# Optimization experiments

Hardware: AMD Instinct MI355X
Metric: run time of the kernel (lower is better)

The kernel has to match this reference:

```python
import jax, jax.numpy as jnp
import numpy as np

HID = 128
NLAYERS = 8
LAT = 32
DIM_IN = 63 + 15 + LAT  # pe(xyz,L=10)=3+60, pe(shift,L=2)=3+12, latent=32 -> 110


def _pe(x, L):
    # NeRF positional encoding, include_input=True, freq-major [sin3,cos3] per freq
    freqs = (2.0 ** jnp.arange(L)).astype(x.dtype)
    xf = x[..., None, :] * freqs[:, None]                      # [..., L, 3]
    sc = jnp.concatenate([jnp.sin(xf), jnp.cos(xf)], axis=-1)  # [..., L, 6]
    return jnp.concatenate([x, sc.reshape(*x.shape[:-1], 6 * L)], axis=-1)


def setup_inputs() -> dict:
    key = jax.random.key(0)
    ks = jax.random.split(key, 24)
    B, P, V = 2, 32768, 5023
    d = {}
    d["pts"] = jax.random.normal(ks[0], (B, P, 3), jnp.float32)
    d["deformed_mesh_pts"] = jax.random.normal(ks[1], (B, V, 3), jnp.float32)
    d["cano_verts"] = jax.random.normal(ks[2], (1, V, 3), jnp.float32)
    d["motion_latent"] = jax.random.normal(ks[3], (B, P, LAT), jnp.float32)
    for i in range(NLAYERS):
        fin = DIM_IN if i == 0 else (DIM_IN + HID if i == NLAYERS // 2 else HID)
        d[f"w{i}"] = jax.random.normal(ks[4 + i], (HID, fin), jnp.float32) / np.sqrt(fin).astype(np.float32)
        d[f"b{i}"] = jnp.zeros((HID,), jnp.float32)
    d["w_out"] = jax.random.normal(ks[20], (3, HID), jnp.float32) * 0.01
    d["b_out"] = jnp.zeros((3,), jnp.float32)
    return d


def reference(pts, deformed_mesh_pts, cano_verts, motion_latent,
              w0, b0, w1, b1, w2, b2, w3, b3, w4, b4, w5, b5, w6, b6, w7, b7,
              w_out, b_out):
    # mesh-guided shift per vertex
    mesh_shift = cano_verts - deformed_mesh_pts                 # [B,V,3]
    # point-to-point NN search (squared euclidean cdist + argmin)
    d2 = ((pts ** 2).sum(-1)[:, :, None]
          + (deformed_mesh_pts ** 2).sum(-1)[:, None, :]
          - 2.0 * jnp.einsum('bpc,bvc->bpv', pts, deformed_mesh_pts))  # [B,P,V]
    d2 = jnp.maximum(d2, 0.0)
    idx = jnp.argmin(d2, axis=-1)                               # [B,P]
    dist = jnp.min(d2, axis=-1)                                 # [B,P]
    weight = jnp.exp(-dist)[..., None]                          # 1/exp(dist)
    gidx = jnp.broadcast_to(idx[:, :, None], idx.shape + (3,))
    gshift = jnp.take_along_axis(mesh_shift, gidx, axis=1) * weight  # [B,P,3]
    # deformation MLP with skip connection at layer 4
    initial = jnp.concatenate([_pe(pts, 10), _pe(gshift, 2), motion_latent], axis=-1)
    ws = [w0, w1, w2, w3, w4, w5, w6, w7]
    bs = [b0, b1, b2, b3, b4, b5, b6, b7]
    x = initial
    last_feat = x
    for i in range(NLAYERS):
        inp = jnp.concatenate([initial, x], axis=-1) if i == NLAYERS // 2 else x
        x = inp @ ws[i].T + bs[i]
        last_feat = x  # pre-activation feature (out_feat_ls[-1])
        x = jax.nn.relu(x)
    mlp_shift = x @ w_out.T + b_out                             # [B,P,3]
    pts_shifts = gshift + mlp_shift
    return pts + pts_shifts, last_feat
```

## Files before the change

kernel.cpp:

```cpp
#include <hip/hip_runtime.h>
#include <math.h>

typedef unsigned short ushort_t;
typedef unsigned int   uint_t;
typedef __attribute__((ext_vector_type(8)))  short bf16x8;
typedef __attribute__((ext_vector_type(16))) float f32x16;

#define NPTS   65536
#define NV     5023
#define LATD   32
#define KF     110
#define FSTR   112

__device__ __forceinline__ ushort_t f2bf(float f) {
  union { float f; unsigned u; } x; x.f = f;
  unsigned r = x.u + 0x7fffu + ((x.u >> 16) & 1u);
  return (ushort_t)(r >> 16);
}
__device__ __forceinline__ float bf2f(ushort_t u) {
  union { unsigned u; float f; } x; x.u = ((unsigned)u) << 16;
  return x.f;
}
__device__ __forceinline__ uint_t packsplit(float v) {
  const ushort_t h = f2bf(v);
  const ushort_t l = f2bf(v - bf2f(h));
  return (uint_t)h | ((uint_t)l << 16);
}


__global__ __launch_bounds__(256, 4) void k_nnfeat(
    const float* __restrict__ pts, const float* __restrict__ dm,
    const float* __restrict__ cano, const float* __restrict__ lat,
    const float* __restrict__ w0, const float* __restrict__ w1,
    const float* __restrict__ w2, const float* __restrict__ w3,
    const float* __restrict__ w4, const float* __restrict__ w5,
    const float* __restrict__ w6, const float* __restrict__ w7,
    uint_t* __restrict__ feat, float* __restrict__ base3,
    ushort_t* __restrict__ wsWh, ushort_t* __restrict__ wsWl)
{
  const int tid = threadIdx.x;

  if (tid < 144) {
    const int e = blockIdx.x * 144 + tid;
    const int p = e >> 14, local = e & 16383;
    const int n = local >> 7, k = local & 127;
    float v;
    if (p == 0)      v = (k < KF) ? w0[n*110 + k] : 0.f;
    else if (p == 1) v = w1[n*128 + k];
    else if (p == 2) v = w2[n*128 + k];
    else if (p == 3) v = w3[n*128 + k];
    else if (p == 4) v = (k < KF) ? w4[n*238 + k] : 0.f;
    else if (p == 5) v = w4[n*238 + KF + k];
    else if (p == 6) v = w5[n*128 + k];
    else if (p == 7) v = w6[n*128 + k];
    else             v = w7[n*128 + k];
    const ushort_t h = f2bf(v);
    wsWh[e] = h;
    wsWl[e] = f2bf(v - bf2f(h));
  }

  __shared__ float4 sV[512];
  __shared__ float  sD[64];
  __shared__ int    sI[64];

  const int lane = tid & 63, w = tid >> 6;
  const int slot = lane >> 4, s = lane & 15;
  const int g0 = blockIdx.x * 64;
  const int b  = blockIdx.x >> 9;
  const float* __restrict__ dmb = dm + b * NV * 3;
  const int pbase = g0 + w*16 + slot*4;

  float px[4], py[4], pz[4], p2[4], bs[4]; int bi[4];
  #pragma unroll
  for (int j = 0; j < 4; ++j) {
    px[j] = pts[(pbase+j)*3+0]; py[j] = pts[(pbase+j)*3+1]; pz[j] = pts[(pbase+j)*3+2];
    p2[j] = fmaf(px[j],px[j], fmaf(py[j],py[j], pz[j]*pz[j]));
    bs[j] = 3.4e38f; bi[j] = 0;
  }

  for (int v0 = 0; v0 < NV; v0 += 512) {
    __syncthreads();
    #pragma unroll
    for (int it = 0; it < 2; ++it) {
      const int i = it*256 + tid;
      const int v = v0 + i;
      float4 t;
      if (v < NV) {
        const float x = dmb[v*3+0], y = dmb[v*3+1], z = dmb[v*3+2];
        t = make_float4(x, y, z, fmaf(x,x, fmaf(y,y, z*z)));
      } else {
        t = make_float4(0.f, 0.f, 0.f, __builtin_inff());
      }
      sV[i] = t;
    }
    __syncthreads();
    #pragma unroll 8
    for (int k = 0; k < 32; ++k) {
      const float4 t = sV[k*16 + s];
      const int vi = v0 + k*16 + s;
      #pragma unroll
      for (int j = 0; j < 4; ++j) {
        const float dot = fmaf(px[j], t.x, fmaf(py[j], t.y, pz[j]*t.z));
        float d2 = fmaf(-2.f, dot, p2[j] + t.w);
        d2 = fmaxf(d2, 0.f);
        if (d2 < bs[j]) { bs[j] = d2; bi[j] = vi; }
      }
    }
  }

  #pragma unroll
  for (int off = 1; off <= 8; off <<= 1) {
    #pragma unroll
    for (int j = 0; j < 4; ++j) {
      const float ob = __shfl_xor(bs[j], off, 64);
      const int   oi = __shfl_xor(bi[j], off, 64);
      const bool take = (ob < bs[j]) || ((ob == bs[j]) && (oi < bi[j]));
      if (take) { bs[j] = ob; bi[j] = oi; }
    }
  }
  if (s == 0) {
    #pragma unroll
    for (int j = 0; j < 4; ++j) {
      sD[w*16 + slot*4 + j] = bs[j];
      sI[w*16 + slot*4 + j] = bi[j];
    }
  }
  __syncthreads();

  const int p = tid & 63, slice = tid >> 6;
  const int g = g0 + p;
  const float wd = sD[p];
  const int   wi = sI[p];

  const float qx = pts[g*3+0], qy = pts[g*3+1], qz = pts[g*3+2];
  const float wgt = expf(-wd);
  const float sx = (cano[wi*3+0] - dmb[wi*3+0]) * wgt;
  const float sy = (cano[wi*3+1] - dmb[wi*3+1]) * wgt;
  const float sz = (cano[wi*3+2] - dmb[wi*3+2]) * wgt;

  uint_t* __restrict__ fr = feat + (size_t)g * FSTR;

  if (slice == 0) {
    base3[g*3+0] = qx + sx; base3[g*3+1] = qy + sy; base3[g*3+2] = qz + sz;
    fr[0] = packsplit(qx); fr[1] = packsplit(qy); fr[2] = packsplit(qz);
    #pragma unroll
    for (int f = 0; f < 3; ++f) {
      const float F = (float)(1 << f);
      float s0,c0,s1,c1,s2,c2;
      sincosf(qx*F,&s0,&c0); sincosf(qy*F,&s1,&c1); sincosf(qz*F,&s2,&c2);
      const int k = 3 + 6*f;
      fr[k+0]=packsplit(s0); fr[k+1]=packsplit(s1); fr[k+2]=packsplit(s2);
      fr[k+3]=packsplit(c0); fr[k+4]=packsplit(c1); fr[k+5]=packsplit(c2);
    }
    fr[110] = 0; fr[111] = 0;
  } else if (slice == 1) {
    #pragma unroll
    for (int f = 3; f < 7; ++f) {
      const float F = (float)(1 << f);
      float s0,c0,s1,c1,s2,c2;
      sincosf(qx*F,&s0,&c0); sincosf(qy*F,&s1,&c1); sincosf(qz*F,&s2,&c2);
      const int k = 3 + 6*f;
      fr[k+0]=packsplit(s0); fr[k+1]=packsplit(s1); fr[k+2]=packsplit(s2);
      fr[k+3]=packsplit(c0); fr[k+4]=packsplit(c1); fr[k+5]=packsplit(c2);
    }
  } else if (slice == 2) {
    #pragma unroll
    for (int f = 7; f < 10; ++f) {
      const float F = (float)(1 << f);
      float s0,c0,s1,c1,s2,c2;
      sincosf(qx*F,&s0,&c0); sincosf(qy*F,&s1,&c1); sincosf(qz*F,&s2,&c2);
      const int k = 3 + 6*f;
      fr[k+0]=packsplit(s0); fr[k+1]=packsplit(s1); fr[k+2]=packsplit(s2);
      fr[k+3]=packsplit(c0); fr[k+4]=packsplit(c1); fr[k+5]=packsplit(c2);
    }
    #pragma unroll
    for (int j = 0; j < 16; ++j) fr[78+j] = packsplit(lat[g*LATD + j]);
  } else {
    fr[63]=packsplit(sx); fr[64]=packsplit(sy); fr[65]=packsplit(sz);
    #pragma unroll
    for (int f = 0; f < 2; ++f) {
      const float F = (float)(1 << f);
      float s0,c0,s1,c1,s2,c2;
      sincosf(sx*F,&s0,&c0); sincosf(sy*F,&s1,&c1); sincosf(sz*F,&s2,&c2);
      const int k = 66 + 6*f;
      fr[k+0]=packsplit(s0); fr[k+1]=packsplit(s1); fr[k+2]=packsplit(s2);
      fr[k+3]=packsplit(c0); fr[k+4]=packsplit(c1); fr[k+5]=packsplit(c2);
    }
    #pragma unroll
    for (int j = 16; j < 32; ++j) fr[78+j] = packsplit(lat[g*LATD + j]);
  }
}


__device__ __forceinline__ void stage_X(uint_t* __restrict__ sX,
    const uint_t* __restrict__ feat, int g0, int tid)
{
  #pragma unroll
  for (int it = 0; it < 14; ++it) {
    const int idx = it*256 + tid;
    const int m = idx / 28, kc = idx - m*28;
    *(uint4*)(sX + m*136 + kc*4) = *(const uint4*)(feat + (size_t)(g0 + m)*FSTR + kc*4);
  }
  const uint4 z = {0,0,0,0};
  #pragma unroll
  for (int it = 0; it < 2; ++it) {
    const int idx = it*256 + tid;
    const int m = idx >> 2, q = idx & 3;
    *(uint4*)(sX + m*136 + 112 + q*4) = z;
  }
}

__device__ __forceinline__ void zero_acc(f32x16 (&acc)[2][2]) {
  #pragma unroll
  for (int i = 0; i < 2; ++i)
    #pragma unroll
    for (int j = 0; j < 2; ++j)
      acc[i][j] = (f32x16)(0.f);
}

__device__ __forceinline__ void mfma_panel(f32x16 (&acc)[2][2],
    const uint_t* __restrict__ sX,
    const ushort_t* __restrict__ gWh, const ushort_t* __restrict__ gWl,
    int mq, int nq, int l31, int lh)
{
  const int kh = lh*8;
  bf16x8 bh[2], bl[2], nbh[2], nbl[2];
  #pragma unroll
  for (int tn = 0; tn < 2; ++tn) {
    const int n = nq*64 + tn*32 + l31;
    bh[tn] = *(const bf16x8*)(gWh + n*128 + kh);
    bl[tn] = *(const bf16x8*)(gWl + n*128 + kh);
  }
  #pragma unroll
  for (int ks = 0; ks < 8; ++ks) {
    const int ko = ks*16 + kh;
    if (ks < 7) {
      #pragma unroll
      for (int tn = 0; tn < 2; ++tn) {
        const int n = nq*64 + tn*32 + l31;
        nbh[tn] = *(const bf16x8*)(gWh + n*128 + ko + 16);
        nbl[tn] = *(const bf16x8*)(gWl + n*128 + ko + 16);
      }
    }
    bf16x8 ah[2], al[2];
    #pragma unroll
    for (int tm = 0; tm < 2; ++tm) {
      const int m = mq*64 + tm*32 + l31;
      const uint4 ua = *(const uint4*)(sX + m*136 + ko);
      const uint4 ub = *(const uint4*)(sX + m*136 + ko + 4);
      union { uint_t u[4]; bf16x8 v; } H, L;
      H.u[0] = (ua.x & 0xffffu) | (ua.y << 16);
      H.u[1] = (ua.z & 0xffffu) | (ua.w << 16);
      H.u[2] = (ub.x & 0xffffu) | (ub.y << 16);
      H.u[3] = (ub.z & 0xffffu) | (ub.w << 16);
      L.u[0] = (ua.x >> 16) | (ua.y & 0xffff0000u);
      L.u[1] = (ua.z >> 16) | (ua.w & 0xffff0000u);
      L.u[2] = (ub.x >> 16) | (ub.y & 0xffff0000u);
      L.u[3] = (ub.z >> 16) | (ub.w & 0xffff0000u);
      ah[tm] = H.v; al[tm] = L.v;
    }
    #pragma unroll
    for (int tm = 0; tm < 2; ++tm)
      #pragma unroll
      for (int tn = 0; tn < 2; ++tn) {
        acc[tm][tn] = __builtin_amdgcn_mfma_f32_32x32x16_bf16(ah[tm], bh[tn], acc[tm][tn], 0,0,0);
        acc[tm][tn] = __builtin_amdgcn_mfma_f32_32x32x16_bf16(al[tm], bh[tn], acc[tm][tn], 0,0,0);
        acc[tm][tn] = __builtin_amdgcn_mfma_f32_32x32x16_bf16(ah[tm], bl[tn], acc[tm][tn], 0,0,0);
      }
    if (ks < 7) {
      #pragma unroll
      for (int tn = 0; tn < 2; ++tn) { bh[tn] = nbh[tn]; bl[tn] = nbl[tn]; }
    }
  }
}

__device__ __forceinline__ void epi_relu(f32x16 (&acc)[2][2], uint_t* __restrict__ sX,
    const float* __restrict__ bias, int mq, int nq, int l31, int lh)
{
  #pragma unroll
  for (int tm = 0; tm < 2; ++tm)
    #pragma unroll
    for (int tn = 0; tn < 2; ++tn) {
      const int n = nq*64 + tn*32 + l31;
      const float bv = bias[n];
      #pragma unroll
      for (int r = 0; r < 16; ++r) {
        const int row = (r & 3) + 8*(r >> 2) + 4*lh;
        const int m = mq*64 + tm*32 + row;
        const float v = fmaxf(acc[tm][tn][r] + bv, 0.f);
        const ushort_t h = f2bf(v);
        const ushort_t l = f2bf(v - bf2f(h));
        sX[m*136 + n] = (uint_t)h | ((uint_t)l << 16);
      }
    }
}

__global__ __launch_bounds__(256, 2) void k_mlp(
    const uint_t* __restrict__ feat, const float* __restrict__ base3,
    const ushort_t* __restrict__ wsWh, const ushort_t* __restrict__ wsWl,
    const float* __restrict__ b0, const float* __restrict__ b1,
    const float* __restrict__ b2, const float* __restrict__ b3,
    const float* __restrict__ b4, const float* __restrict__ b5,
    const float* __restrict__ b6, const float* __restrict__ b7,
    const float* __restrict__ w_out, const float* __restrict__ b_out,
    float* __restrict__ out)
{
  __shared__ __align__(16) uint_t sX[128*136];
  __shared__ float sB[8*128 + 384 + 4];

  const int tid  = threadIdx.x;
  const int lane = tid & 63, wid = tid >> 6;
  const int l31 = lane & 31, lh = lane >> 5;
  const int mq = wid & 1, nq = wid >> 1;
  const int g0 = blockIdx.x * 128;

  f32x16 acc[2][2];

  stage_X(sX, feat, g0, tid);
  {
    const float* bs[8] = {b0,b1,b2,b3,b4,b5,b6,b7};
    if (tid < 128) {
      #pragma unroll
      for (int l = 0; l < 8; ++l) sB[l*128 + tid] = bs[l][tid];
    }
    for (int i = tid; i < 384; i += 256) sB[1024 + i] = w_out[i];
    if (tid < 3) sB[1408 + tid] = b_out[tid];
  }
  __syncthreads();

  zero_acc(acc);
  mfma_panel(acc, sX, wsWh + 0, wsWl + 0, mq, nq, l31, lh);
  __syncthreads();
  epi_relu(acc, sX, sB + 0, mq, nq, l31, lh);

  for (int l = 1; l <= 3; ++l) {
    __syncthreads();
    zero_acc(acc);
    mfma_panel(acc, sX, wsWh + l*16384, wsWl + l*16384, mq, nq, l31, lh);
    __syncthreads();
    epi_relu(acc, sX, sB + l*128, mq, nq, l31, lh);
  }

  __syncthreads();
  zero_acc(acc);
  mfma_panel(acc, sX, wsWh + 5*16384, wsWl + 5*16384, mq, nq, l31, lh);
  __syncthreads();
  stage_X(sX, feat, g0, tid);
  __syncthreads();
  mfma_panel(acc, sX, wsWh + 4*16384, wsWl + 4*16384, mq, nq, l31, lh);
  __syncthreads();
  epi_relu(acc, sX, sB + 4*128, mq, nq, l31, lh);

  for (int l = 5; l <= 6; ++l) {
    __syncthreads();
    zero_acc(acc);
    mfma_panel(acc, sX, wsWh + (l+1)*16384, wsWl + (l+1)*16384, mq, nq, l31, lh);
    __syncthreads();
    epi_relu(acc, sX, sB + l*128, mq, nq, l31, lh);
  }

  __syncthreads();
  zero_acc(acc);
  mfma_panel(acc, sX, wsWh + 8*16384, wsWl + 8*16384, mq, nq, l31, lh);

  float* __restrict__ out1 = out + (size_t)NPTS*3;
  #pragma unroll
  for (int tm = 0; tm < 2; ++tm)
    #pragma unroll
    for (int tn = 0; tn < 2; ++tn) {
      const int n = nq*64 + tn*32 + l31;
      const float bv = sB[7*128 + n];
      #pragma unroll
      for (int r = 0; r < 16; ++r) {
        const int row = (r & 3) + 8*(r >> 2) + 4*lh;
        const int m = mq*64 + tm*32 + row;
        const float v = acc[tm][tn][r] + bv;
        out1[(size_t)(g0 + m)*128 + n] = v;
        acc[tm][tn][r] = fmaxf(v, 0.f);
      }
    }

  __syncthreads();
  float* __restrict__ sF = (float*)sX;
  #pragma unroll
  for (int tm = 0; tm < 2; ++tm)
    #pragma unroll
    for (int tn = 0; tn < 2; ++tn) {
      const int n = nq*64 + tn*32 + l31;
      #pragma unroll
      for (int r = 0; r < 16; ++r) {
        const int row = (r & 3) + 8*(r >> 2) + 4*lh;
        const int m = mq*64 + tm*32 + row;
        sF[m*132 + n] = acc[tm][tn][r];
      }
    }
  __syncthreads();

  for (int pair = tid; pair < 384; pair += 256) {
    const int m = pair / 3, c = pair - m*3;
    const float* __restrict__ xr = sF + m*132;
    const float* __restrict__ wc = sB + 1024 + c*128;
    float a = 0.f;
    #pragma unroll 8
    for (int k = 0; k < 128; ++k) a = fmaf(xr[k], wc[k], a);
    const int g = g0 + m;
    out[g*3 + c] = base3[g*3 + c] + a + sB[1408 + c];
  }
}

extern "C" void kernel_launch(void* const* d_in, const int* in_sizes, int n_in,
                              void* d_out, int out_size, void* d_ws, size_t ws_size,
                              hipStream_t stream)
{
  const float* pts  = (const float*)d_in[0];
  const float* dm   = (const float*)d_in[1];
  const float* cano = (const float*)d_in[2];
  const float* lat  = (const float*)d_in[3];
  const float* w[8]; const float* b[8];
  for (int i = 0; i < 8; ++i) {
    w[i] = (const float*)d_in[4 + 2*i];
    b[i] = (const float*)d_in[5 + 2*i];
  }
  const float* w_out = (const float*)d_in[20];
  const float* b_out = (const float*)d_in[21];
  float* out = (float*)d_out;

  uint_t*   feat  = (uint_t*)d_ws;
  float*    base3 = (float*)((char*)d_ws + (size_t)NPTS*FSTR*4);
  ushort_t* wsWh  = (ushort_t*)((char*)base3 + (size_t)NPTS*3*4);
  ushort_t* wsWl  = wsWh + 147456;

  k_nnfeat<<<1024, 256, 0, stream>>>(pts, dm, cano, lat,
      w[0],w[1],w[2],w[3],w[4],w[5],w[6],w[7], feat, base3, wsWh, wsWl);
  k_mlp<<<NPTS/128, 256, 0, stream>>>(feat, base3, wsWh, wsWl,
      b[0],b[1],b[2],b[3],b[4],b[5],b[6],b[7], w_out, b_out, out);
}
```

Before: 275.5 us.

## Keep MLP activations in registers per wave instead of shared-memory round trips

```diff
diff --git a/kernel.cpp b/kernel.cpp
--- a/kernel.cpp
+++ b/kernel.cpp
@@ -192,107 +192,105 @@
 }
 
 
-__device__ __forceinline__ void stage_X(uint_t* __restrict__ sX,
-    const uint_t* __restrict__ feat, int g0, int tid)
-{
-  #pragma unroll
-  for (int it = 0; it < 14; ++it) {
-    const int idx = it*256 + tid;
-    const int m = idx / 28, kc = idx - m*28;
-    *(uint4*)(sX + m*136 + kc*4) = *(const uint4*)(feat + (size_t)(g0 + m)*FSTR + kc*4);
-  }
-  const uint4 z = {0,0,0,0};
-  #pragma unroll
-  for (int it = 0; it < 2; ++it) {
-    const int idx = it*256 + tid;
-    const int m = idx >> 2, q = idx & 3;
-    *(uint4*)(sX + m*136 + 112 + q*4) = z;
-  }
-}
-
-__device__ __forceinline__ void zero_acc(f32x16 (&acc)[2][2]) {
-  #pragma unroll
-  for (int i = 0; i < 2; ++i)
-    #pragma unroll
-    for (int j = 0; j < 2; ++j)
-      acc[i][j] = (f32x16)(0.f);
-}
-
-__device__ __forceinline__ void mfma_panel(f32x16 (&acc)[2][2],
-    const uint_t* __restrict__ sX,
-    const ushort_t* __restrict__ gWh, const ushort_t* __restrict__ gWl,
-    int mq, int nq, int l31, int lh)
-{
-  const int kh = lh*8;
-  bf16x8 bh[2], bl[2], nbh[2], nbl[2];
-  #pragma unroll
-  for (int tn = 0; tn < 2; ++tn) {
-    const int n = nq*64 + tn*32 + l31;
-    bh[tn] = *(const bf16x8*)(gWh + n*128 + kh);
-    bl[tn] = *(const bf16x8*)(gWl + n*128 + kh);
-  }
+union U4 { uint_t u[4]; bf16x8 v; };
+
+__device__ __forceinline__ void zero4(f32x16 (&a)[4]) {
+  #pragma unroll
+  for (int i = 0; i < 4; ++i) a[i] = (f32x16)(0.f);
+}
+
+__device__ __forceinline__ void load_feat_frags(
+    const uint_t* __restrict__ fr, bf16x8 (&Xh)[8], bf16x8 (&Xl)[8], int lh)
+{
+  #pragma unroll
+  for (int ks = 0; ks < 7; ++ks) {
+    const int k0 = ks*16 + lh*8;
+    const uint4 ua = *(const uint4*)(fr + k0);
+    const uint4 ub = *(const uint4*)(fr + k0 + 4);
+    U4 H, L;
+    H.u[0] = (ua.x & 0xffffu) | (ua.y << 16);
+    H.u[1] = (ua.z & 0xffffu) | (ua.w << 16);
+    H.u[2] = (ub.x & 0xffffu) | (ub.y << 16);
+    H.u[3] = (ub.z & 0xffffu) | (ub.w << 16);
+    L.u[0] = (ua.x >> 16) | (ua.y & 0xffff0000u);
+    L.u[1] = (ua.z >> 16) | (ua.w & 0xffff0000u);
+    L.u[2] = (ub.x >> 16) | (ub.y & 0xffff0000u);
+    L.u[3] = (ub.z >> 16) | (ub.w & 0xffff0000u);
+    Xh[ks] = H.v; Xl[ks] = L.v;
+  }
+}
+
+template<int NKS>
+__device__ __forceinline__ void run_panel(f32x16 (&acc)[4],
+    const ushort_t* __restrict__ Wh, const ushort_t* __restrict__ Wl,
+    const bf16x8 (&Xh)[8], const bf16x8 (&Xl)[8], int l31, int lh)
+{
+  #pragma unroll
+  for (int ks = 0; ks < NKS; ++ks) {
+    const int k0 = ks*16 + lh*8;
+    bf16x8 wh[4], wl[4];
+    #pragma unroll
+    for (int tn = 0; tn < 4; ++tn) {
+      const int n = tn*32 + l31;
+      wh[tn] = *(const bf16x8*)(Wh + n*128 + k0);
+      wl[tn] = *(const bf16x8*)(Wl + n*128 + k0);
+    }
+    #pragma unroll
+    for (int tn = 0; tn < 4; ++tn) {
+      acc[tn] = __builtin_amdgcn_mfma_f32_32x32x16_bf16(wh[tn], Xh[ks], acc[tn], 0,0,0);
+      acc[tn] = __builtin_amdgcn_mfma_f32_32x32x16_bf16(wl[tn], Xh[ks], acc[tn], 0,0,0);
+      acc[tn] = __builtin_amdgcn_mfma_f32_32x32x16_bf16(wh[tn], Xl[ks], acc[tn], 0,0,0);
+    }
+  }
+}
+
+__device__ __forceinline__ void bias_relu(f32x16 (&acc)[4],
+    const float* __restrict__ bias, int lh)
+{
+  #pragma unroll
+  for (int tn = 0; tn < 4; ++tn)
+    #pragma unroll
+    for (int b = 0; b < 4; ++b) {
+      const float4 b4 = *(const float4*)(bias + tn*32 + 8*b + 4*lh);
+      acc[tn][4*b+0] = fmaxf(acc[tn][4*b+0] + b4.x, 0.f);
+      acc[tn][4*b+1] = fmaxf(acc[tn][4*b+1] + b4.y, 0.f);
+      acc[tn][4*b+2] = fmaxf(acc[tn][4*b+2] + b4.z, 0.f);
+      acc[tn][4*b+3] = fmaxf(acc[tn][4*b+3] + b4.w, 0.f);
+    }
+}
+
+__device__ __forceinline__ void build_frags(const f32x16 (&acc)[4],
+    bf16x8 (&Xh)[8], bf16x8 (&Xl)[8], int lh)
+{
   #pragma unroll
   for (int ks = 0; ks < 8; ++ks) {
-    const int ko = ks*16 + kh;
-    if (ks < 7) {
-      #pragma unroll
-      for (int tn = 0; tn < 2; ++tn) {
-        const int n = nq*64 + tn*32 + l31;
-        nbh[tn] = *(const bf16x8*)(gWh + n*128 + ko + 16);
-        nbl[tn] = *(const bf16x8*)(gWl + n*128 + ko + 16);
-      }
-    }
-    bf16x8 ah[2], al[2];
-    #pragma unroll
-    for (int tm = 0; tm < 2; ++tm) {
-      const int m = mq*64 + tm*32 + l31;
-      const uint4 ua = *(const uint4*)(sX + m*136 + ko);
-      const uint4 ub = *(const uint4*)(sX + m*136 + ko + 4);
-      union { uint_t u[4]; bf16x8 v; } H, L;
-      H.u[0] = (ua.x & 0xffffu) | (ua.y << 16);
-      H.u[1] = (ua.z & 0xffffu) | (ua.w << 16);
-      H.u[2] = (ub.x & 0xffffu) | (ub.y << 16);
-      H.u[3] = (ub.z & 0xffffu) | (ub.w << 16);
-      L.u[0] = (ua.x >> 16) | (ua.y & 0xffff0000u);
-      L.u[1] = (ua.z >> 16) | (ua.w & 0xffff0000u);
-      L.u[2] = (ub.x >> 16) | (ub.y & 0xffff0000u);
-      L.u[3] = (ub.z >> 16) | (ub.w & 0xffff0000u);
-      ah[tm] = H.v; al[tm] = L.v;
-    }
-    #pragma unroll
-    for (int tm = 0; tm < 2; ++tm)
-      #pragma unroll
-      for (int tn = 0; tn < 2; ++tn) {
-        acc[tm][tn] = __builtin_amdgcn_mfma_f32_32x32x16_bf16(ah[tm], bh[tn], acc[tm][tn], 0,0,0);
-        acc[tm][tn] = __builtin_amdgcn_mfma_f32_32x32x16_bf16(al[tm], bh[tn], acc[tm][tn], 0,0,0);
-        acc[tm][tn] = __builtin_amdgcn_mfma_f32_32x32x16_bf16(ah[tm], bl[tn], acc[tm][tn], 0,0,0);
-      }
-    if (ks < 7) {
-      #pragma unroll
-      for (int tn = 0; tn < 2; ++tn) { bh[tn] = nbh[tn]; bl[tn] = nbl[tn]; }
-    }
-  }
-}
-
-__device__ __forceinline__ void epi_relu(f32x16 (&acc)[2][2], uint_t* __restrict__ sX,
-    const float* __restrict__ bias, int mq, int nq, int l31, int lh)
-{
-  #pragma unroll
-  for (int tm = 0; tm < 2; ++tm)
-    #pragma unroll
-    for (int tn = 0; tn < 2; ++tn) {
-      const int n = nq*64 + tn*32 + l31;
-      const float bv = bias[n];
-      #pragma unroll
-      for (int r = 0; r < 16; ++r) {
-        const int row = (r & 3) + 8*(r >> 2) + 4*lh;
-        const int m = mq*64 + tm*32 + row;
-        const float v = fmaxf(acc[tm][tn][r] + bv, 0.f);
-        const ushort_t h = f2bf(v);
-        const ushort_t l = f2bf(v - bf2f(h));
-        sX[m*136 + n] = (uint_t)h | ((uint_t)l << 16);
-      }
-    }
+    const int tn = ks >> 1;
+    const int rb = 8*(ks & 1);
+    const float f0 = acc[tn][rb+0], f1 = acc[tn][rb+1];
+    const float f2 = acc[tn][rb+2], f3 = acc[tn][rb+3];
+    const float f4 = acc[tn][rb+4], f5 = acc[tn][rb+5];
+    const float f6 = acc[tn][rb+6], f7 = acc[tn][rb+7];
+    const ushort_t h0=f2bf(f0), h1=f2bf(f1), h2=f2bf(f2), h3=f2bf(f3);
+    const ushort_t h4=f2bf(f4), h5=f2bf(f5), h6=f2bf(f6), h7=f2bf(f7);
+    const uint_t hA0 = (uint_t)h0 | ((uint_t)h1 << 16);
+    const uint_t hA1 = (uint_t)h2 | ((uint_t)h3 << 16);
+    const uint_t hB0 = (uint_t)h4 | ((uint_t)h5 << 16);
+    const uint_t hB1 = (uint_t)h6 | ((uint_t)h7 << 16);
+    const uint_t lA0 = (uint_t)f2bf(f0 - bf2f(h0)) | ((uint_t)f2bf(f1 - bf2f(h1)) << 16);
+    const uint_t lA1 = (uint_t)f2bf(f2 - bf2f(h2)) | ((uint_t)f2bf(f3 - bf2f(h3)) << 16);
+    const uint_t lB0 = (uint_t)f2bf(f4 - bf2f(h4)) | ((uint_t)f2bf(f5 - bf2f(h5)) << 16);
+    const uint_t lB1 = (uint_t)f2bf(f6 - bf2f(h6)) | ((uint_t)f2bf(f7 - bf2f(h7)) << 16);
+    const uint_t sh0 = lh ? hA0 : hB0, sh1 = lh ? hA1 : hB1;
+    const uint_t sl0 = lh ? lA0 : lB0, sl1 = lh ? lA1 : lB1;
+    const uint_t rh0 = __shfl_xor(sh0, 32, 64), rh1 = __shfl_xor(sh1, 32, 64);
+    const uint_t rl0 = __shfl_xor(sl0, 32, 64), rl1 = __shfl_xor(sl1, 32, 64);
+    U4 H, L;
+    H.u[0] = lh ? rh0 : hA0;  H.u[1] = lh ? rh1 : hA1;
+    H.u[2] = lh ? hB0 : rh0;  H.u[3] = lh ? hB1 : rh1;
+    L.u[0] = lh ? rl0 : lA0;  L.u[1] = lh ? rl1 : lA1;
+    L.u[2] = lh ? lB0 : rl0;  L.u[3] = lh ? lB1 : rl1;
+    Xh[ks] = H.v; Xl[ks] = L.v;
+  }
 }
 
 __global__ __launch_bounds__(256, 2) void k_mlp(
@@ -305,106 +303,127 @@
     const float* __restrict__ w_out, const float* __restrict__ b_out,
     float* __restrict__ out)
 {
-  __shared__ __align__(16) uint_t sX[128*136];
-  __shared__ float sB[8*128 + 384 + 4];
+  __shared__ __align__(16) float sF[4][32*132];
+  __shared__ __align__(16) float sB[8*128 + 384 + 4];
 
   const int tid  = threadIdx.x;
   const int lane = tid & 63, wid = tid >> 6;
   const int l31 = lane & 31, lh = lane >> 5;
-  const int mq = wid & 1, nq = wid >> 1;
-  const int g0 = blockIdx.x * 128;
-
-  f32x16 acc[2][2];
-
-  stage_X(sX, feat, g0, tid);
+  const int p0 = blockIdx.x * 128 + wid * 32;
+
   {
-    const float* bs[8] = {b0,b1,b2,b3,b4,b5,b6,b7};
+    const float* bsp[8] = {b0,b1,b2,b3,b4,b5,b6,b7};
     if (tid < 128) {
       #pragma unroll
-      for (int l = 0; l < 8; ++l) sB[l*128 + tid] = bs[l][tid];
+      for (int l = 0; l < 8; ++l) sB[l*128 + tid] = bsp[l][tid];
     }
     for (int i = tid; i < 384; i += 256) sB[1024 + i] = w_out[i];
     if (tid < 3) sB[1408 + tid] = b_out[tid];
   }
   __syncthreads();
 
-  zero_acc(acc);
-  mfma_panel(acc, sX, wsWh + 0, wsWl + 0, mq, nq, l31, lh);
-  __syncthreads();
-  epi_relu(acc, sX, sB + 0, mq, nq, l31, lh);
-
-  for (int l = 1; l <= 3; ++l) {
-    __syncthreads();
-    zero_acc(acc);
-    mfma_panel(acc, sX, wsWh + l*16384, wsWl + l*16384, mq, nq, l31, lh);
-    __syncthreads();
-    epi_relu(acc, sX, sB + l*128, mq, nq, l31, lh);
-  }
-
-  __syncthreads();
-  zero_acc(acc);
-  mfma_panel(acc, sX, wsWh + 5*16384, wsWl + 5*16384, mq, nq, l31, lh);
-  __syncthreads();
-  stage_X(sX, feat, g0, tid);
-  __syncthreads();
-  mfma_panel(acc, sX, wsWh + 4*16384, wsWl + 4*16384, mq, nq, l31, lh);
-  __syncthreads();
-  epi_relu(acc, sX, sB + 4*128, mq, nq, l31, lh);
-
-  for (int l = 5; l <= 6; ++l) {
-    __syncthreads();
-    zero_acc(acc);
-    mfma_panel(acc, sX, wsWh + (l+1)*16384, wsWl + (l+1)*16384, mq, nq, l31, lh);
-    __syncthreads();
-    epi_relu(acc, sX, sB + l*128, mq, nq, l31, lh);
-  }
-
-  __syncthreads();
-  zero_acc(acc);
-  mfma_panel(acc, sX, wsWh + 8*16384, wsWl + 8*16384, mq, nq, l31, lh);
-
-  float* __restrict__ out1 = out + (size_t)NPTS*3;
-  #pragma unroll
-  for (int tm = 0; tm < 2; ++tm)
-    #pragma unroll
-    for (int tn = 0; tn < 2; ++tn) {
-      const int n = nq*64 + tn*32 + l31;
-      const float bv = sB[7*128 + n];
+  const uint_t* __restrict__ fr = feat + (size_t)(p0 + l31) * FSTR;
+
+  bf16x8 Xh[8], Xl[8];
+  f32x16 acc[4];
+
+  load_feat_frags(fr, Xh, Xl, lh);
+  zero4(acc);
+  run_panel<7>(acc, wsWh, wsWl, Xh, Xl, l31, lh);
+  bias_relu(acc, sB, lh);
+  build_frags(acc, Xh, Xl, lh);
+
+  {
+    const ushort_t* ph = wsWh + 16384;
+    const ushort_t* pl = wsWl + 16384;
+    const float*    pb = sB + 128;
+    #pragma unroll 1
+    for (int l = 0; l < 3; ++l) {
+      zero4(acc);
+      run_panel<8>(acc, ph, pl, Xh, Xl, l31, lh);
+      bias_relu(acc, pb, lh);
+      build_frags(acc, Xh, Xl, lh);
+      ph += 16384; pl += 16384; pb += 128;
+    }
+  }
+
+  zero4(acc);
+  run_panel<8>(acc, wsWh + 5*16384, wsWl + 5*16384, Xh, Xl, l31, lh);
+  load_feat_frags(fr, Xh, Xl, lh);
+  run_panel<7>(acc, wsWh + 4*16384, wsWl + 4*16384, Xh, Xl, l31, lh);
+  bias_relu(acc, sB + 4*128, lh);
+  build_frags(acc, Xh, Xl, lh);
+
+  {
+    const ushort_t* ph = wsWh + 6*16384;
+    const ushort_t* pl = wsWl + 6*16384;
+    const float*    pb = sB + 5*128;
+    #pragma unroll 1
+    for (int l = 0; l < 2; ++l) {
+      zero4(acc);
+      run_panel<8>(acc, ph, pl, Xh, Xl, l31, lh);
+      bias_relu(acc, pb, lh);
+      build_frags(acc, Xh, Xl, lh);
+      ph += 16384; pl += 16384; pb += 128;
+    }
+  }
+
+  zero4(acc);
+  run_panel<8>(acc, wsWh + 8*16384, wsWl + 8*16384, Xh, Xl, l31, lh);
+
+  float* __restrict__ sFw = &sF[wid][0];
+  #pragma unroll
+  for (int tn = 0; tn < 4; ++tn)
+    #pragma unroll
+    for (int b = 0; b < 4; ++b) {
+      const int n0 = tn*32 + 8*b + 4*lh;
+      const float4 bv = *(const float4*)(sB + 7*128 + n0);
+      const float v0 = acc[tn][4*b+0] + bv.x;
+      const float v1 = acc[tn][4*b+1] + bv.y;
+      const float v2 = acc[tn][4*b+2] + bv.z;
+      const float v3 = acc[tn][4*b+3] + bv.w;
+      *(float4*)(sFw + l31*132 + n0) = make_float4(v0, v1, v2, v3);
+      acc[tn][4*b+0] = fmaxf(v0, 0.f);
+      acc[tn][4*b+1] = fmaxf(v1, 0.f);
+      acc[tn][4*b+2] = fmaxf(v2, 0.f);
+      acc[tn][4*b+3] = fmaxf(v3, 0.f);
+    }
+
+  asm volatile("s_waitcnt lgkmcnt(0)" ::: "memory");
+  __builtin_amdgcn_sched_barrier(0);
+
+  float* __restrict__ out1 = out + (size_t)NPTS * 3;
+  #pragma unroll
+  for (int i = 0; i < 16; ++i) {
+    const int idx = i*64 + lane;
+    const int p = idx >> 5, q = idx & 31;
+    const float4 v = *(const float4*)(sFw + p*132 + q*4);
+    *(float4*)(out1 + (size_t)(p0 + p)*128 + q*4) = v;
+  }
+
+  float dotc[3];
+  #pragma unroll
+  for (int c = 0; c < 3; ++c) {
+    float a = 0.f;
+    #pragma unroll
+    for (int tn = 0; tn < 4; ++tn)
       #pragma unroll
-      for (int r = 0; r < 16; ++r) {
-        const int row = (r & 3) + 8*(r >> 2) + 4*lh;
-        const int m = mq*64 + tm*32 + row;
-        const float v = acc[tm][tn][r] + bv;
-        out1[(size_t)(g0 + m)*128 + n] = v;
-        acc[tm][tn][r] = fmaxf(v, 0.f);
+      for (int b = 0; b < 4; ++b) {
+        const int n0 = tn*32 + 8*b + 4*lh;
+        const float4 w4 = *(const float4*)(sB + 1024 + c*128 + n0);
+        a = fmaf(acc[tn][4*b+0], w4.x, a);
+        a = fmaf(acc[tn][4*b+1], w4.y, a);
+        a = fmaf(acc[tn][4*b+2], w4.z, a);
+        a = fmaf(acc[tn][4*b+3], w4.w, a);
       }
-    }
-
-  __syncthreads();
-  float* __restrict__ sF = (float*)sX;
-  #pragma unroll
-  for (int tm = 0; tm < 2; ++tm)
-    #pragma unroll
-    for (int tn = 0; tn < 2; ++tn) {
-      const int n = nq*64 + tn*32 + l31;
-      #pragma unroll
-      for (int r = 0; r < 16; ++r) {
-        const int row = (r & 3) + 8*(r >> 2) + 4*lh;
-        const int m = mq*64 + tm*32 + row;
-        sF[m*132 + n] = acc[tm][tn][r];
-      }
-    }
-  __syncthreads();
-
-  for (int pair = tid; pair < 384; pair += 256) {
-    const int m = pair / 3, c = pair - m*3;
-    const float* __restrict__ xr = sF + m*132;
-    const float* __restrict__ wc = sB + 1024 + c*128;
-    float a = 0.f;
-    #pragma unroll 8
-    for (int k = 0; k < 128; ++k) a = fmaf(xr[k], wc[k], a);
-    const int g = g0 + m;
-    out[g*3 + c] = base3[g*3 + c] + a + sB[1408 + c];
+    a += __shfl_xor(a, 32, 64);
+    dotc[c] = a;
+  }
+  if (lh == 0) {
+    const int g = p0 + l31;
+    #pragma unroll
+    for (int c = 0; c < 3; ++c)
+      out[g*3 + c] = base3[g*3 + c] + dotc[c] + sB[1408 + c];
   }
 }
 
```

Measured after the change: 321.0 us. 16.5% more time.
